# Performance work log

Hardware: AMD Instinct MI355X
Metric: run time of the kernel (lower is better)

## Reference

```python
import jax, jax.numpy as jnp
from jax import lax
import numpy as np

# --- module hyperparams (match S2_GaussianBlur(nr=2048, nc=2048, kernelSize=10, scale=2, RealData=False)) ---
NR, NC, KS, SCALE = 2048, 2048, 10, 2
MTF = np.array([0.38, 0.34, 0.34, 0.26, 0.22, 0.23])  # mtf[[4,5,6,8,10,11]] for scale==2
C = len(MTF)


def _gaussian_kernels():
    # sigmas = scale * sqrt(-2 ln(mtf) / pi^2)
    sigmas = SCALE * np.sqrt(-2.0 * np.log(MTF) / np.pi ** 2)  # (C,)
    end = int(KS / 2) - 0.5
    coords = np.arange(-end, end + 1.0, 1.0)  # (KS,) = [-4.5, ..., 4.5]
    g1 = np.exp(-coords[None, :] ** 2 / (2.0 * sigmas[:, None] ** 2)) / (
        sigmas[:, None] * np.sqrt(2.0 * np.pi))  # (C,KS)
    k = g1[:, :, None] * g1[:, None, :]  # separable outer product -> (C,KS,KS)
    k = k / k.sum(axis=(1, 2), keepdims=True)
    return k.astype(np.float32)


_KERNELS = jnp.asarray(_gaussian_kernels())  # (C,KS,KS), fixed buffers (requires_grad=False)

# Offsets replicating: circular pad by (nr//2, nc//2), conv with full-image kernel B
# (Gaussian patch placed at [row_start:row_end, col_start:col_end], then flipped both
# axes), crop [0:-1, 0:-1].  This collapses exactly to a circular cross-correlation
# with the flipped KSxKS patch at a fixed shift:
_MIDL, _MIDC = NR // 2, NC // 2
_EB = -int(SCALE / 2)
_ROW_START = int(_MIDL - KS / 2 + _EB)
_COL_START = int(_MIDC - KS / 2 + _EB)
_PAD_T = _MIDL + _ROW_START + KS - NR  # left/top circular pad (=4 here)
_PAD_L = _MIDC + _COL_START + KS - NC
assert 0 <= _PAD_T < KS and 0 <= _PAD_L < KS


def setup_inputs() -> dict:
    key = jax.random.key(0)
    x = jax.random.normal(key, (1, C, NR, NC), dtype=jnp.float32)
    return {"x": x}


def _blur(x):
    # circular (wrap) pad so every output pixel sees its KSxKS circular neighborhood
    xpad = jnp.pad(x, ((0, 0), (0, 0), (_PAD_T, KS - 1 - _PAD_T), (_PAD_L, KS - 1 - _PAD_L)), mode="wrap")
    # flipped Gaussian patch (the full-image kernel B was flipped on both axes)
    w = _KERNELS[:, ::-1, ::-1][:, None, :, :]  # (C,1,KS,KS), depthwise
    return lax.conv_general_dilated(
        xpad, w, window_strides=(1, 1), padding="VALID",
        dimension_numbers=("NCHW", "OIHW", "NCHW"), feature_group_count=C)


def reference(x):
    return _blur(x)  # (1,C,NR,NC)
```

## Files before the change

kernel.cpp:

```cpp
#include <hip/hip_runtime.h>
#include <math.h>

constexpr int C  = 6;
constexpr int NR = 2048;
constexpr int NC = 2048;
constexpr int KS = 10;
constexpr int PAD = 4;

constexpr int TX = 64;
constexpr int TY = 64;
constexpr int RAW_W = TX + KS - 1;
constexpr int RAW_H = TY + KS - 1;
constexpr int RAW_STRIDE = 77;

__device__ const double MTFd[C] = {0.38, 0.34, 0.34, 0.26, 0.22, 0.23};

__global__ __launch_bounds__(256)
void s2_gaussian_blur_kernel(const float* __restrict__ x, float* __restrict__ out)
{
    __shared__ float  raw[RAW_H * RAW_STRIDE];
    __shared__ float  Ht[RAW_H * TX];
    __shared__ double gd[KS];

    const int tid = threadIdx.x;
    const int c   = blockIdx.z;
    const int i0  = blockIdx.y * TY;
    const int j0  = blockIdx.x * TX;

    const float* xc = x   + (size_t)c * NR * NC;
    float*       oc = out + (size_t)c * NR * NC;

    if (tid < KS) {
        double mtf   = MTFd[c];
        double sigma = 2.0 * sqrt(-2.0 * log(mtf) / (3.14159265358979323846 * 3.14159265358979323846));
        double cd    = -4.5 + (double)tid;
        gd[tid] = exp(-cd * cd / (2.0 * sigma * sigma));
    }

    for (int idx = tid; idx < RAW_H * RAW_W; idx += 256) {
        int r  = idx / RAW_W;
        int cc = idx - r * RAW_W;
        int gr = (i0 + r  + NR - PAD) & (NR - 1);
        int gc = (j0 + cc + NC - PAD) & (NC - 1);
        raw[r * RAW_STRIDE + cc] = xc[(size_t)gr * NC + gc];
    }
    __syncthreads();

    float w[KS];
    {
        double s = 0.0;
        #pragma unroll
        for (int d = 0; d < KS; ++d) s += gd[d];
        double inv = 1.0 / s;
        #pragma unroll
        for (int d = 0; d < KS; ++d) w[d] = (float)(gd[d] * inv);
    }

    for (int item = tid; item < RAW_H * (TX / 8); item += 256) {
        int r = item >> 3;
        int g = item & 7;
        int base = r * RAW_STRIDE + g * 8;
        float v[17];
        #pragma unroll
        for (int k = 0; k < 17; ++k) v[k] = raw[base + k];
        #pragma unroll
        for (int o = 0; o < 8; ++o) {
            float acc = 0.f;
            #pragma unroll
            for (int d = 0; d < KS; ++d) acc = fmaf(w[d], v[o + d], acc);
            Ht[r * TX + g * 8 + o] = acc;
        }
    }
    __syncthreads();

    const int jj  = tid & 63;
    const int rg0 = tid >> 6;
    for (int rg = rg0; rg < TY / 8; rg += 4) {
        int base = rg * 8 * TX + jj;
        float v[17];
        #pragma unroll
        for (int k = 0; k < 17; ++k) v[k] = Ht[base + k * TX];
        #pragma unroll
        for (int o = 0; o < 8; ++o) {
            float acc = 0.f;
            #pragma unroll
            for (int d = 0; d < KS; ++d) acc = fmaf(w[d], v[o + d], acc);
            oc[(size_t)(i0 + rg * 8 + o) * NC + (j0 + jj)] = acc;
        }
    }
}

extern "C" void kernel_launch(void* const* d_in, const int* in_sizes, int n_in,
                              void* d_out, int out_size, void* d_ws, size_t ws_size,
                              hipStream_t stream) {
    const float* x = (const float*)d_in[0];
    float* out = (float*)d_out;
    dim3 grid(NC / TX, NR / TY, C);
    dim3 block(256);
    s2_gaussian_blur_kernel<<<grid, block, 0, stream>>>(x, out);
}
```

Before: 198.0 us.

## Fuse horizontal pass with global loads, vectorize accesses, compute weights in fp32

The raw shared-memory staging tile is gone. Each thread now reads its 17-element row window straight from global memory, using float4 loads for interior tiles and wrap-indexed scalar loads at the edges, and writes the horizontal result to shared memory as float4. The vertical pass is remapped so each thread computes a 4x4 output block from float4 shared reads and stores float4 to global. Gaussian weights are computed per thread in fp32 instead of in fp64 through shared memory. Unaligned float4 global loads (offset -4 is 16B-aligned here) and fp32 weight rounding may differ slightly from the reference.

```diff
diff --git a/kernel.cpp b/kernel.cpp
--- a/kernel.cpp
+++ b/kernel.cpp
@@ -9,18 +9,14 @@
 
 constexpr int TX = 64;
 constexpr int TY = 64;
-constexpr int RAW_W = TX + KS - 1;
-constexpr int RAW_H = TY + KS - 1;
-constexpr int RAW_STRIDE = 77;
+constexpr int HT_H = TY + KS - 1;
 
-__device__ const double MTFd[C] = {0.38, 0.34, 0.34, 0.26, 0.22, 0.23};
+__device__ __constant__ float MTFf[C] = {0.38f, 0.34f, 0.34f, 0.26f, 0.22f, 0.23f};
 
 __global__ __launch_bounds__(256)
 void s2_gaussian_blur_kernel(const float* __restrict__ x, float* __restrict__ out)
 {
-    __shared__ float  raw[RAW_H * RAW_STRIDE];
-    __shared__ float  Ht[RAW_H * TX];
-    __shared__ double gd[KS];
+    __shared__ float Ht[HT_H * TX];
 
     const int tid = threadIdx.x;
     const int c   = blockIdx.z;
@@ -30,62 +26,84 @@
     const float* xc = x   + (size_t)c * NR * NC;
     float*       oc = out + (size_t)c * NR * NC;
 
-    if (tid < KS) {
-        double mtf   = MTFd[c];
-        double sigma = 2.0 * sqrt(-2.0 * log(mtf) / (3.14159265358979323846 * 3.14159265358979323846));
-        double cd    = -4.5 + (double)tid;
-        gd[tid] = exp(-cd * cd / (2.0 * sigma * sigma));
+    float w[KS];
+    {
+        float mtf    = MTFf[c];
+        float sig    = 2.0f * sqrtf(-2.0f * logf(mtf) / (float)(M_PI * M_PI));
+        float inv2s2 = 1.0f / (2.0f * sig * sig);
+        float s = 0.0f;
+        #pragma unroll
+        for (int d = 0; d < KS; ++d) {
+            float cd = -4.5f + (float)d;
+            w[d] = expf(-cd * cd * inv2s2);
+            s += w[d];
+        }
+        #pragma unroll
+        for (int d = 0; d < KS; ++d) w[d] /= s;
     }
 
-    for (int idx = tid; idx < RAW_H * RAW_W; idx += 256) {
-        int r  = idx / RAW_W;
-        int cc = idx - r * RAW_W;
-        int gr = (i0 + r  + NR - PAD) & (NR - 1);
-        int gc = (j0 + cc + NC - PAD) & (NC - 1);
-        raw[r * RAW_STRIDE + cc] = xc[(size_t)gr * NC + gc];
+    const bool interior = (blockIdx.x >= 1) && (blockIdx.x <= (NC / TX) - 2);
+
+    for (int item = tid; item < HT_H * (TX / 8); item += 256) {
+        const int r = item >> 3;
+        const int g = item & 7;
+        const int gr = (i0 + r - PAD + NR) & (NR - 1);
+        const float* row = xc + (size_t)gr * NC;
+
+        float v[17];
+        if (interior) {
+            const float4* p = (const float4*)(row + j0 + 8 * g - PAD);
+            float4 a = p[0], b = p[1], d2 = p[2], d3 = p[3];
+            v[0]=a.x;  v[1]=a.y;  v[2]=a.z;  v[3]=a.w;
+            v[4]=b.x;  v[5]=b.y;  v[6]=b.z;  v[7]=b.w;
+            v[8]=d2.x; v[9]=d2.y; v[10]=d2.z; v[11]=d2.w;
+            v[12]=d3.x; v[13]=d3.y; v[14]=d3.z; v[15]=d3.w;
+            v[16] = row[j0 + 8 * g + 12];
+        } else {
+            #pragma unroll
+            for (int k = 0; k < 17; ++k)
+                v[k] = row[(j0 + 8 * g + k - PAD + NC) & (NC - 1)];
+        }
+
+        float acc[8];
+        #pragma unroll
+        for (int o = 0; o < 8; ++o) {
+            float a = 0.0f;
+            #pragma unroll
+            for (int d = 0; d < KS; ++d) a = fmaf(w[d], v[o + d], a);
+            acc[o] = a;
+        }
+        float4* q = (float4*)&Ht[r * TX + 8 * g];
+        q[0] = make_float4(acc[0], acc[1], acc[2], acc[3]);
+        q[1] = make_float4(acc[4], acc[5], acc[6], acc[7]);
     }
+
     __syncthreads();
 
-    float w[KS];
     {
-        double s = 0.0;
+        const int cg = tid & 15;
+        const int rg = tid >> 4;
+        float acc[4][4] = {{0.f}};
+
         #pragma unroll
-        for (int d = 0; d < KS; ++d) s += gd[d];
-        double inv = 1.0 / s;
+        for (int k = 0; k < 13; ++k) {
+            float4 h = *(const float4*)&Ht[(rg * 4 + k) * TX + cg * 4];
+            #pragma unroll
+            for (int o = 0; o < 4; ++o) {
+                const int d = k - o;
+                if (d >= 0 && d < KS) {
+                    acc[o][0] = fmaf(w[d], h.x, acc[o][0]);
+                    acc[o][1] = fmaf(w[d], h.y, acc[o][1]);
+                    acc[o][2] = fmaf(w[d], h.z, acc[o][2]);
+                    acc[o][3] = fmaf(w[d], h.w, acc[o][3]);
+                }
+            }
+        }
+
         #pragma unroll
-        for (int d = 0; d < KS; ++d) w[d] = (float)(gd[d] * inv);
-    }
-
-    for (int item = tid; item < RAW_H * (TX / 8); item += 256) {
-        int r = item >> 3;
-        int g = item & 7;
-        int base = r * RAW_STRIDE + g * 8;
-        float v[17];
-        #pragma unroll
-        for (int k = 0; k < 17; ++k) v[k] = raw[base + k];
-        #pragma unroll
-        for (int o = 0; o < 8; ++o) {
-            float acc = 0.f;
-            #pragma unroll
-            for (int d = 0; d < KS; ++d) acc = fmaf(w[d], v[o + d], acc);
-            Ht[r * TX + g * 8 + o] = acc;
-        }
-    }
-    __syncthreads();
-
-    const int jj  = tid & 63;
-    const int rg0 = tid >> 6;
-    for (int rg = rg0; rg < TY / 8; rg += 4) {
-        int base = rg * 8 * TX + jj;
-        float v[17];
-        #pragma unroll
-        for (int k = 0; k < 17; ++k) v[k] = Ht[base + k * TX];
-        #pragma unroll
-        for (int o = 0; o < 8; ++o) {
-            float acc = 0.f;
-            #pragma unroll
-            for (int d = 0; d < KS; ++d) acc = fmaf(w[d], v[o + d], acc);
-            oc[(size_t)(i0 + rg * 8 + o) * NC + (j0 + jj)] = acc;
+        for (int o = 0; o < 4; ++o) {
+            float4* q = (float4*)&oc[(size_t)(i0 + rg * 4 + o) * NC + (j0 + cg * 4)];
+            *q = make_float4(acc[o][0], acc[o][1], acc[o][2], acc[o][3]);
         }
     }
 }
```

Result: slower. 218.7 us (+10.5%).

## Halve tile height, compute float weights in registers, vectorize intermediate stores

Applied to the files above, without the earlier changes.

Tile height drops from 64 to 32 rows, so each thread handles a single 8-row group in the vertical pass and the grid doubles. Shared memory per block shrinks, and launch bounds now request 6 blocks per CU to raise occupancy. The Gaussian weights are computed per thread in float from constant memory instead of in double via shared memory, which removes a shared array and a dependency on the barrier. Horizontal-pass results are written to shared memory with float4 stores. The cost is more halo reloading per output, since 9 extra rows are fetched for every 32 instead of every 64, plus small float-versus-double differences in the weights.

```diff
diff --git a/kernel.cpp b/kernel.cpp
--- a/kernel.cpp
+++ b/kernel.cpp
@@ -1,26 +1,25 @@
 #include <hip/hip_runtime.h>
 #include <math.h>
 
-constexpr int C  = 6;
-constexpr int NR = 2048;
-constexpr int NC = 2048;
-constexpr int KS = 10;
+constexpr int C   = 6;
+constexpr int NR  = 2048;
+constexpr int NC  = 2048;
+constexpr int KS  = 10;
 constexpr int PAD = 4;
 
 constexpr int TX = 64;
-constexpr int TY = 64;
+constexpr int TY = 32;
 constexpr int RAW_W = TX + KS - 1;
 constexpr int RAW_H = TY + KS - 1;
 constexpr int RAW_STRIDE = 77;
 
-__device__ const double MTFd[C] = {0.38, 0.34, 0.34, 0.26, 0.22, 0.23};
+__device__ __constant__ float MTFf[C] = {0.38f, 0.34f, 0.34f, 0.26f, 0.22f, 0.23f};
 
-__global__ __launch_bounds__(256)
+__global__ __launch_bounds__(256, 6)
 void s2_gaussian_blur_kernel(const float* __restrict__ x, float* __restrict__ out)
 {
-    __shared__ float  raw[RAW_H * RAW_STRIDE];
-    __shared__ float  Ht[RAW_H * TX];
-    __shared__ double gd[KS];
+    __shared__ float raw[RAW_H * RAW_STRIDE];
+    __shared__ float Ht[RAW_H * TX];
 
     const int tid = threadIdx.x;
     const int c   = blockIdx.z;
@@ -30,31 +29,30 @@
     const float* xc = x   + (size_t)c * NR * NC;
     float*       oc = out + (size_t)c * NR * NC;
 
-    if (tid < KS) {
-        double mtf   = MTFd[c];
-        double sigma = 2.0 * sqrt(-2.0 * log(mtf) / (3.14159265358979323846 * 3.14159265358979323846));
-        double cd    = -4.5 + (double)tid;
-        gd[tid] = exp(-cd * cd / (2.0 * sigma * sigma));
+    float w[KS];
+    {
+        float mtf    = MTFf[c];
+        float sig    = 2.0f * sqrtf(-2.0f * logf(mtf) / (float)(M_PI * M_PI));
+        float inv2s2 = 1.0f / (2.0f * sig * sig);
+        float s = 0.0f;
+        #pragma unroll
+        for (int d = 0; d < KS; ++d) {
+            float cd = -4.5f + (float)d;
+            w[d] = expf(-cd * cd * inv2s2);
+            s += w[d];
+        }
+        #pragma unroll
+        for (int d = 0; d < KS; ++d) w[d] /= s;
     }
 
     for (int idx = tid; idx < RAW_H * RAW_W; idx += 256) {
         int r  = idx / RAW_W;
         int cc = idx - r * RAW_W;
-        int gr = (i0 + r  + NR - PAD) & (NR - 1);
-        int gc = (j0 + cc + NC - PAD) & (NC - 1);
+        int gr = (i0 + r  - PAD + NR) & (NR - 1);
+        int gc = (j0 + cc - PAD + NC) & (NC - 1);
         raw[r * RAW_STRIDE + cc] = xc[(size_t)gr * NC + gc];
     }
     __syncthreads();
-
-    float w[KS];
-    {
-        double s = 0.0;
-        #pragma unroll
-        for (int d = 0; d < KS; ++d) s += gd[d];
-        double inv = 1.0 / s;
-        #pragma unroll
-        for (int d = 0; d < KS; ++d) w[d] = (float)(gd[d] * inv);
-    }
 
     for (int item = tid; item < RAW_H * (TX / 8); item += 256) {
         int r = item >> 3;
@@ -63,29 +61,33 @@
         float v[17];
         #pragma unroll
         for (int k = 0; k < 17; ++k) v[k] = raw[base + k];
+        float acc[8];
         #pragma unroll
         for (int o = 0; o < 8; ++o) {
-            float acc = 0.f;
+            float a = 0.f;
             #pragma unroll
-            for (int d = 0; d < KS; ++d) acc = fmaf(w[d], v[o + d], acc);
-            Ht[r * TX + g * 8 + o] = acc;
+            for (int d = 0; d < KS; ++d) a = fmaf(w[d], v[o + d], a);
+            acc[o] = a;
         }
+        float4* q = (float4*)&Ht[r * TX + g * 8];
+        q[0] = make_float4(acc[0], acc[1], acc[2], acc[3]);
+        q[1] = make_float4(acc[4], acc[5], acc[6], acc[7]);
     }
     __syncthreads();
 
-    const int jj  = tid & 63;
-    const int rg0 = tid >> 6;
-    for (int rg = rg0; rg < TY / 8; rg += 4) {
+    {
+        const int jj = tid & 63;
+        const int rg = tid >> 6;
         int base = rg * 8 * TX + jj;
         float v[17];
         #pragma unroll
         for (int k = 0; k < 17; ++k) v[k] = Ht[base + k * TX];
         #pragma unroll
         for (int o = 0; o < 8; ++o) {
-            float acc = 0.f;
+            float a = 0.f;
             #pragma unroll
-            for (int d = 0; d < KS; ++d) acc = fmaf(w[d], v[o + d], acc);
-            oc[(size_t)(i0 + rg * 8 + o) * NC + (j0 + jj)] = acc;
+            for (int d = 0; d < KS; ++d) a = fmaf(w[d], v[o + d], a);
+            oc[(size_t)(i0 + rg * 8 + o) * NC + (j0 + jj)] = a;
         }
     }
 }
```

New measurement: 218.9 us. 10.6% more time.
